# Optimization experiments

Hardware: AMD Instinct MI355X
Metric: run time of the kernel (lower is better)

Reference implementation:

```python
import jax, jax.numpy as jnp
import numpy as np

NUM_PATCHES_SIDE = 32
LOCAL_RADIUS = 3.0


def _build_non_local_mask():
    # coords of each patch on the grid, matching torch.meshgrid(indexing='ij')
    h = np.arange(NUM_PATCHES_SIDE)
    hh, ww = np.meshgrid(h, h, indexing='ij')
    coors = np.stack([hh, ww], axis=0).astype(np.float32)  # (2, H, W)
    coors = coors.reshape(2, -1).T                          # (n, 2)
    dist = np.linalg.norm(coors[:, None, :] - coors[None, :, :], axis=-1)
    return jnp.asarray(dist > LOCAL_RADIUS)                 # (n, n) bool


def setup_inputs() -> dict:
    key = jax.random.key(0)
    b, n, l, d = 8, NUM_PATCHES_SIDE * NUM_PATCHES_SIDE, 6, 512
    levels = jax.random.normal(key, (b, n, l, d), dtype=jnp.float32)
    non_local_mask = _build_non_local_mask()
    return {"levels": levels, "non_local_mask": non_local_mask}


def reference(levels, non_local_mask):
    b, n, l, d = levels.shape
    # F.normalize(levels, dim=-1): x / max(||x||, eps)
    norm = jnp.linalg.norm(levels, axis=-1, keepdims=True)
    k = levels / jnp.maximum(norm, 1e-12)
    # scores per level: (b, l, n, n)
    sim = jnp.einsum('bild,bjld->blij', levels, k) * (d ** -0.5)
    max_neg = -jnp.finfo(sim.dtype).max
    sim = jnp.where(non_local_mask[None, None, :, :], max_neg, sim)
    attn = jax.nn.softmax(sim, axis=-1)
    out = jnp.einsum('blij,bjld->bild', attn, levels)
    return out
```

## Files before the change

kernel.cpp:

```cpp
#include <hip/hip_runtime.h>
#include <math.h>

#define NPS 32
#define NN  (NPS*NPS)
#define LL  6
#define DD  512
#define ROWSPB (NN*LL)
#define BIAS 576

#define INV_SQRT_D 0.044194173824159216f
#define LOG2E      1.4426950408889634f
#define KLOG       (INV_SQRT_D * LOG2E)

__device__ __forceinline__ float half_sum32(float x) {
    int t;
    t = __builtin_amdgcn_update_dpp(0, __float_as_int(x), 0xB1, 0xF, 0xF, true);
    x += __int_as_float(t);
    t = __builtin_amdgcn_update_dpp(0, __float_as_int(x), 0x4E, 0xF, 0xF, true);
    x += __int_as_float(t);
    t = __builtin_amdgcn_update_dpp(0, __float_as_int(x), 0x141, 0xF, 0xF, true);
    x += __int_as_float(t);
    t = __builtin_amdgcn_update_dpp(0, __float_as_int(x), 0x140, 0xF, 0xF, true);
    x += __int_as_float(t);
    x += __int_as_float(__builtin_amdgcn_ds_swizzle(__float_as_int(x), 0x401F));
    return x;
}

__device__ __forceinline__ float wave_sum_bcast(float x) {
    x = half_sum32(x);
    x += __shfl_xor(x, 32, 64);
    return x;
}

__global__ __launch_bounds__(256) void ca_norm2(const float* __restrict__ levels,
                                                float* __restrict__ cws,
                                                float* __restrict__ mws, int rows) {
    int tid  = threadIdx.x;
    int lane = tid & 63;
    int sl   = lane & 31;
    int grp  = lane >> 5;
    int w = ((int)blockIdx.x * 4 + (tid >> 6)) * 2 + grp;
    if (w >= rows) return;
    const float4* x4 = (const float4*)(levels + (unsigned)(w * DD));
    float4 a0 = x4[sl], a1 = x4[sl+32], a2 = x4[sl+64], a3 = x4[sl+96];
    float s2 = a0.x*a0.x + a0.y*a0.y + a0.z*a0.z + a0.w*a0.w
             + a1.x*a1.x + a1.y*a1.y + a1.z*a1.z + a1.w*a1.w
             + a2.x*a2.x + a2.y*a2.y + a2.z*a2.z + a2.w*a2.w
             + a3.x*a3.x + a3.y*a3.y + a3.z*a3.z + a3.w*a3.w;
    s2 = half_sum32(s2);
    if (sl == 0) {
        float r = __frsqrt_rn(s2);
        cws[w] = KLOG * r;
        mws[w] = KLOG * s2 * r;
    }
}

__global__ __launch_bounds__(256) void ca_fused3(const float* __restrict__ levels,
                                                 const float* __restrict__ cws,
                                                 const float* __restrict__ mws,
                                                 float* __restrict__ out, int rows) {
    constexpr int dhA[14] = {-3,-2,-2,-1,-1,-1, 0, 0, 0, 1, 1, 2, 2, 2};
    constexpr int dwA[14] = { 0,-1, 1,-2, 0, 2,-2, 1, 3,-1, 1,-2, 0, 2};
    constexpr int dhB[14] = {-2,-2,-2,-1,-1, 0, 0, 0, 1, 1, 1, 2, 2, 3};
    constexpr int dwB[14] = {-2, 0, 2,-1, 1,-3,-1, 2,-2, 0, 2,-1, 1, 0};

    unsigned bk    = blockIdx.x;
    unsigned chunk = gridDim.x >> 3;
    unsigned vb    = (bk & 7) * chunk + (bk >> 3);

    int tid  = threadIdx.x;
    int lane = tid & 63;
    int sl   = lane & 31;
    bool hi  = lane >= 32;

    int b  = (int)(vb / 1536u);
    int r1 = (int)(vb - (unsigned)b * 1536u);
    int pg = r1 / 6;
    int l  = r1 - pg * 6;
    int p  = __builtin_amdgcn_readfirstlane(pg * 4 + (tid >> 6));
    int w  = __builtin_amdgcn_readfirstlane(b * ROWSPB + p * LL + l);
    if (w >= rows) return;
    int ph = p >> 5;
    int pw = p & 31;

    const float4* xi4 = (const float4*)(levels + (size_t)w * DD);
    float4 a0 = xi4[sl], a1 = xi4[sl+32], a2 = xi4[sl+64], a3 = xi4[sl+96];

    float m2 = mws[w];

    float  lsum = 0.0f;
    float4 c0 = make_float4(0.f,0.f,0.f,0.f);
    float4 c1 = make_float4(0.f,0.f,0.f,0.f);
    float4 c2 = make_float4(0.f,0.f,0.f,0.f);
    float4 c3 = make_float4(0.f,0.f,0.f,0.f);

    const char* lvb   = (const char*)levels + ((long long)w - BIAS) * (DD * 4);
    const char* cwb   = (const char*)cws    + ((long long)w - BIAS) * 4;

    #pragma unroll
    for (int t = 0; t < 14; ++t) {
        int hA = ph + dhA[t], wA = pw + dwA[t];
        int hB = ph + dhB[t], wB = pw + dwB[t];
        bool vA = ((unsigned)hA < NPS) && ((unsigned)wA < NPS);
        bool vB = ((unsigned)hB < NPS) && ((unsigned)wB < NPS);
        if (vA | vB) {
            int roffA = vA ? (dhA[t] * NPS + dwA[t]) * LL : 0;
            int roffB = vB ? (dhB[t] * NPS + dwB[t]) * LL : 0;
            int offA  = (roffA + BIAS) * (DD * 4);
            int offB  = (roffB + BIAS) * (DD * 4);
            int off   = hi ? offB : offA;
            const float4* bp = (const float4*)(lvb + off);
            float4 b0 = bp[sl], b1 = bp[sl+32], b2 = bp[sl+64], b3 = bp[sl+96];
            float cj = *(const float*)(cwb + (off >> 9));

            float d;
            d = a0.x * b0.x;
            d = fmaf(a0.y, b0.y, d); d = fmaf(a0.z, b0.z, d); d = fmaf(a0.w, b0.w, d);
            d = fmaf(a1.x, b1.x, d); d = fmaf(a1.y, b1.y, d); d = fmaf(a1.z, b1.z, d);
            d = fmaf(a1.w, b1.w, d);
            d = fmaf(a2.x, b2.x, d); d = fmaf(a2.y, b2.y, d); d = fmaf(a2.z, b2.z, d);
            d = fmaf(a2.w, b2.w, d);
            d = fmaf(a3.x, b3.x, d); d = fmaf(a3.y, b3.y, d); d = fmaf(a3.z, b3.z, d);
            d = fmaf(a3.w, b3.w, d);
            d = half_sum32(d);

            float pr = __builtin_amdgcn_exp2f(fmaf(d, cj, -m2));
            bool myv = hi ? vB : vA;
            pr = myv ? pr : 0.0f;
            lsum += pr;
            c0.x = fmaf(pr, b0.x, c0.x); c0.y = fmaf(pr, b0.y, c0.y);
            c0.z = fmaf(pr, b0.z, c0.z); c0.w = fmaf(pr, b0.w, c0.w);
            c1.x = fmaf(pr, b1.x, c1.x); c1.y = fmaf(pr, b1.y, c1.y);
            c1.z = fmaf(pr, b1.z, c1.z); c1.w = fmaf(pr, b1.w, c1.w);
            c2.x = fmaf(pr, b2.x, c2.x); c2.y = fmaf(pr, b2.y, c2.y);
            c2.z = fmaf(pr, b2.z, c2.z); c2.w = fmaf(pr, b2.w, c2.w);
            c3.x = fmaf(pr, b3.x, c3.x); c3.y = fmaf(pr, b3.y, c3.y);
            c3.z = fmaf(pr, b3.z, c3.z); c3.w = fmaf(pr, b3.w, c3.w);
        }
    }

    lsum += __shfl_xor(lsum, 32, 64);
    c0.x += __shfl_xor(c0.x, 32, 64); c0.y += __shfl_xor(c0.y, 32, 64);
    c0.z += __shfl_xor(c0.z, 32, 64); c0.w += __shfl_xor(c0.w, 32, 64);
    c1.x += __shfl_xor(c1.x, 32, 64); c1.y += __shfl_xor(c1.y, 32, 64);
    c1.z += __shfl_xor(c1.z, 32, 64); c1.w += __shfl_xor(c1.w, 32, 64);
    c2.x += __shfl_xor(c2.x, 32, 64); c2.y += __shfl_xor(c2.y, 32, 64);
    c2.z += __shfl_xor(c2.z, 32, 64); c2.w += __shfl_xor(c2.w, 32, 64);
    c3.x += __shfl_xor(c3.x, 32, 64); c3.y += __shfl_xor(c3.y, 32, 64);
    c3.z += __shfl_xor(c3.z, 32, 64); c3.w += __shfl_xor(c3.w, 32, 64);

    lsum += 1.0f;
    c0.x += a0.x; c0.y += a0.y; c0.z += a0.z; c0.w += a0.w;
    c1.x += a1.x; c1.y += a1.y; c1.z += a1.z; c1.w += a1.w;
    c2.x += a2.x; c2.y += a2.y; c2.z += a2.z; c2.w += a2.w;
    c3.x += a3.x; c3.y += a3.y; c3.z += a3.z; c3.w += a3.w;

    if (!hi) {
        float inv = 1.0f / lsum;
        float4* o4 = (float4*)(out + (size_t)w * DD);
        o4[sl]    = make_float4(c0.x*inv, c0.y*inv, c0.z*inv, c0.w*inv);
        o4[sl+32] = make_float4(c1.x*inv, c1.y*inv, c1.z*inv, c1.w*inv);
        o4[sl+64] = make_float4(c2.x*inv, c2.y*inv, c2.z*inv, c2.w*inv);
        o4[sl+96] = make_float4(c3.x*inv, c3.y*inv, c3.z*inv, c3.w*inv);
    }
}

__global__ __launch_bounds__(256) void ca_fallback(const float* __restrict__ levels,
                                                   float* __restrict__ out, int rows) {
    constexpr int dh[28] = {-3,-2,-2,-2,-2,-2,-1,-1,-1,-1,-1, 0, 0, 0, 0, 0, 0,
                             1, 1, 1, 1, 1, 2, 2, 2, 2, 2, 3};
    constexpr int dw[28] = { 0,-2,-1, 0, 1, 2,-2,-1, 0, 1, 2,-3,-2,-1, 1, 2, 3,
                            -2,-1, 0, 1, 2,-2,-1, 0, 1, 2, 0};
    unsigned bk    = blockIdx.x;
    unsigned chunk = gridDim.x >> 3;
    unsigned vb    = (bk & 7) * chunk + (bk >> 3);
    int w = __builtin_amdgcn_readfirstlane((int)(vb * 4 + (threadIdx.x >> 6)));
    if (w >= rows) return;
    int lane = threadIdx.x & 63;
    int i  = (w / LL) % NN;
    int ph = i >> 5, pw = i & 31;
    const float4* xi4 = (const float4*)(levels + (size_t)w * DD);
    float4 a0 = xi4[lane], a1 = xi4[lane + 64];
    float s2i = a0.x*a0.x + a0.y*a0.y + a0.z*a0.z + a0.w*a0.w
              + a1.x*a1.x + a1.y*a1.y + a1.z*a1.z + a1.w*a1.w;
    s2i = wave_sum_bcast(s2i);
    float m2 = __fsqrt_rn(s2i) * KLOG;
    float lsum = 1.0f;
    float acc0=a0.x, acc1=a0.y, acc2=a0.z, acc3=a0.w;
    float acc4=a1.x, acc5=a1.y, acc6=a1.z, acc7=a1.w;
    #pragma unroll
    for (int t = 0; t < 28; ++t) {
        int hh = ph + dh[t], ww = pw + dw[t];
        if ((unsigned)hh < (unsigned)NPS && (unsigned)ww < (unsigned)NPS) {
            int jrow = w + (dh[t] * NPS + dw[t]) * LL;
            const float4* xj4 = (const float4*)(levels + (size_t)jrow * DD);
            float4 b0 = xj4[lane], b1 = xj4[lane + 64];
            float d = a0.x * b0.x;
            d = fmaf(a0.y, b0.y, d); d = fmaf(a0.z, b0.z, d); d = fmaf(a0.w, b0.w, d);
            d = fmaf(a1.x, b1.x, d); d = fmaf(a1.y, b1.y, d); d = fmaf(a1.z, b1.z, d);
            d = fmaf(a1.w, b1.w, d);
            d = wave_sum_bcast(d);
            float q2 = b0.x*b0.x + b0.y*b0.y + b0.z*b0.z + b0.w*b0.w
                     + b1.x*b1.x + b1.y*b1.y + b1.z*b1.z + b1.w*b1.w;
            q2 = wave_sum_bcast(q2);
            float cj = KLOG * __frsqrt_rn(q2);
            float p = __builtin_amdgcn_exp2f(fmaf(d, cj, -m2));
            lsum += p;
            acc0 = fmaf(p, b0.x, acc0); acc1 = fmaf(p, b0.y, acc1);
            acc2 = fmaf(p, b0.z, acc2); acc3 = fmaf(p, b0.w, acc3);
            acc4 = fmaf(p, b1.x, acc4); acc5 = fmaf(p, b1.y, acc5);
            acc6 = fmaf(p, b1.z, acc6); acc7 = fmaf(p, b1.w, acc7);
        }
    }
    float inv = 1.0f / lsum;
    float4* o4 = (float4*)(out + (size_t)w * DD);
    o4[lane]      = make_float4(acc0*inv, acc1*inv, acc2*inv, acc3*inv);
    o4[lane + 64] = make_float4(acc4*inv, acc5*inv, acc6*inv, acc7*inv);
}

extern "C" void kernel_launch(void* const* d_in, const int* in_sizes, int n_in,
                              void* d_out, int out_size, void* d_ws, size_t ws_size,
                              hipStream_t stream) {
    const float* levels = (const float*)d_in[0];
    float* out = (float*)d_out;

    int rows = in_sizes[0] / DD;

    if (d_ws && ws_size >= (size_t)rows * 2 * sizeof(float)) {
        float* cws = (float*)d_ws;
        float* mws = cws + rows;
        int blocks1 = (rows + 7) / 8;
        ca_norm2<<<blocks1, 256, 0, stream>>>(levels, cws, mws, rows);
        int blocks2 = rows / 4;
        ca_fused3<<<blocks2, 256, 0, stream>>>(levels, cws, mws, out, rows);
    } else {
        int blocks = (rows + 3) / 4;
        ca_fallback<<<blocks, 256, 0, stream>>>(levels, out, rows);
    }
}
```

Measured before the change: 254.2 us.

## Process two horizontally adjacent query patches per wave to share neighbor loads

Each wave now handles two adjacent query rows (patches p0 and p0+1) instead of one. The neighbor loop iterates over the union of both patches' local windows, so each loaded neighbor vector is used for both queries when it lies in both windows. This halves the block count and is meant to cut redundant global/L2 reads of neighbor rows. In exchange it doubles the accumulator register footprint, which may lower occupancy, and it adds a rows%48 guard on the fast path.

```diff
diff --git a/kernel.cpp b/kernel.cpp
--- a/kernel.cpp
+++ b/kernel.cpp
@@ -30,6 +30,21 @@
     x = half_sum32(x);
     x += __shfl_xor(x, 32, 64);
     return x;
+}
+
+__device__ __forceinline__ float dot16(const float4& a0, const float4& a1,
+                                       const float4& a2, const float4& a3,
+                                       const float4& b0, const float4& b1,
+                                       const float4& b2, const float4& b3) {
+    float d = a0.x * b0.x;
+    d = fmaf(a0.y, b0.y, d); d = fmaf(a0.z, b0.z, d); d = fmaf(a0.w, b0.w, d);
+    d = fmaf(a1.x, b1.x, d); d = fmaf(a1.y, b1.y, d); d = fmaf(a1.z, b1.z, d);
+    d = fmaf(a1.w, b1.w, d);
+    d = fmaf(a2.x, b2.x, d); d = fmaf(a2.y, b2.y, d); d = fmaf(a2.z, b2.z, d);
+    d = fmaf(a2.w, b2.w, d);
+    d = fmaf(a3.x, b3.x, d); d = fmaf(a3.y, b3.y, d); d = fmaf(a3.z, b3.z, d);
+    d = fmaf(a3.w, b3.w, d);
+    return d;
 }
 
 __global__ __launch_bounds__(256) void ca_norm2(const float* __restrict__ levels,
@@ -43,10 +58,7 @@
     if (w >= rows) return;
     const float4* x4 = (const float4*)(levels + (unsigned)(w * DD));
     float4 a0 = x4[sl], a1 = x4[sl+32], a2 = x4[sl+64], a3 = x4[sl+96];
-    float s2 = a0.x*a0.x + a0.y*a0.y + a0.z*a0.z + a0.w*a0.w
-             + a1.x*a1.x + a1.y*a1.y + a1.z*a1.z + a1.w*a1.w
-             + a2.x*a2.x + a2.y*a2.y + a2.z*a2.z + a2.w*a2.w
-             + a3.x*a3.x + a3.y*a3.y + a3.z*a3.z + a3.w*a3.w;
+    float s2 = dot16(a0,a1,a2,a3, a0,a1,a2,a3);
     s2 = half_sum32(s2);
     if (sl == 0) {
         float r = __frsqrt_rn(s2);
@@ -55,14 +67,16 @@
     }
 }
 
-__global__ __launch_bounds__(256) void ca_fused3(const float* __restrict__ levels,
+__global__ __launch_bounds__(256) void ca_fused4(const float* __restrict__ levels,
                                                  const float* __restrict__ cws,
                                                  const float* __restrict__ mws,
                                                  float* __restrict__ out, int rows) {
-    constexpr int dhA[14] = {-3,-2,-2,-1,-1,-1, 0, 0, 0, 1, 1, 2, 2, 2};
-    constexpr int dwA[14] = { 0,-1, 1,-2, 0, 2,-2, 1, 3,-1, 1,-2, 0, 2};
-    constexpr int dhB[14] = {-2,-2,-2,-1,-1, 0, 0, 0, 1, 1, 1, 2, 2, 3};
-    constexpr int dwB[14] = {-2, 0, 2,-1, 1,-3,-1, 2,-2, 0, 2,-1, 1, 0};
+    constexpr int NIT = 18;
+    constexpr int typ [NIT] = { 2, 2, 2, 2, 2, 2, 2, 2, 2, 2,  0, 0, 0, 0,  1, 1, 1, 1};
+    constexpr int dhA_[NIT] = {-2,-2,-1,-1, 0, 0, 1, 1, 2, 2, -3,-2,-1, 0, -3,-2,-1, 0};
+    constexpr int duA_[NIT] = {-1, 0,-1, 0,-2,-1,-1, 0,-1, 0,  0,-2,-2,-3,  1, 3, 3, 0};
+    constexpr int dhB_[NIT] = {-2,-2,-1,-1, 0, 0, 1, 1, 2, 2,  0, 1, 2, 3,  0, 1, 2, 3};
+    constexpr int duB_[NIT] = { 1, 2, 1, 2, 2, 3, 1, 2, 1, 2,  1,-2,-2, 0,  4, 3, 3, 1};
 
     unsigned bk    = blockIdx.x;
     unsigned chunk = gridDim.x >> 3;
@@ -73,96 +87,116 @@
     int sl   = lane & 31;
     bool hi  = lane >= 32;
 
-    int b  = (int)(vb / 1536u);
-    int r1 = (int)(vb - (unsigned)b * 1536u);
+    int b  = (int)(vb / 768u);
+    int r1 = (int)(vb - (unsigned)b * 768u);
     int pg = r1 / 6;
     int l  = r1 - pg * 6;
-    int p  = __builtin_amdgcn_readfirstlane(pg * 4 + (tid >> 6));
-    int w  = __builtin_amdgcn_readfirstlane(b * ROWSPB + p * LL + l);
-    if (w >= rows) return;
-    int ph = p >> 5;
-    int pw = p & 31;
-
-    const float4* xi4 = (const float4*)(levels + (size_t)w * DD);
-    float4 a0 = xi4[sl], a1 = xi4[sl+32], a2 = xi4[sl+64], a3 = xi4[sl+96];
-
-    float m2 = mws[w];
-
-    float  lsum = 0.0f;
-    float4 c0 = make_float4(0.f,0.f,0.f,0.f);
-    float4 c1 = make_float4(0.f,0.f,0.f,0.f);
-    float4 c2 = make_float4(0.f,0.f,0.f,0.f);
-    float4 c3 = make_float4(0.f,0.f,0.f,0.f);
-
-    const char* lvb   = (const char*)levels + ((long long)w - BIAS) * (DD * 4);
-    const char* cwb   = (const char*)cws    + ((long long)w - BIAS) * 4;
+    int p0 = pg * 8 + ((tid >> 6) << 1);
+    int w0 = __builtin_amdgcn_readfirstlane(b * ROWSPB + p0 * LL + l);
+    if (w0 >= rows) return;
+    int ph  = p0 >> 5;
+    int pw0 = p0 & 31;
+
+    const float4* x0 = (const float4*)(levels + (size_t)w0 * DD);
+    const float4* x1 = x0 + (DD / 4) * LL;
+    float4 a00 = x0[sl], a01 = x0[sl+32], a02 = x0[sl+64], a03 = x0[sl+96];
+    float4 a10 = x1[sl], a11 = x1[sl+32], a12 = x1[sl+64], a13 = x1[sl+96];
+
+    float m20 = mws[w0];
+    float m21 = mws[w0 + LL];
+
+    float  lsum0 = 0.0f, lsum1 = 0.0f;
+    float4 c00 = make_float4(0,0,0,0), c01 = make_float4(0,0,0,0);
+    float4 c02 = make_float4(0,0,0,0), c03 = make_float4(0,0,0,0);
+    float4 c10 = make_float4(0,0,0,0), c11 = make_float4(0,0,0,0);
+    float4 c12 = make_float4(0,0,0,0), c13 = make_float4(0,0,0,0);
+
+    const char* lvb = (const char*)levels + ((long long)w0 - BIAS) * (DD * 4);
+    const char* cwb = (const char*)cws    + ((long long)w0 - BIAS) * 4;
 
     #pragma unroll
-    for (int t = 0; t < 14; ++t) {
-        int hA = ph + dhA[t], wA = pw + dwA[t];
-        int hB = ph + dhB[t], wB = pw + dwB[t];
-        bool vA = ((unsigned)hA < NPS) && ((unsigned)wA < NPS);
-        bool vB = ((unsigned)hB < NPS) && ((unsigned)wB < NPS);
-        if (vA | vB) {
-            int roffA = vA ? (dhA[t] * NPS + dwA[t]) * LL : 0;
-            int roffB = vB ? (dhB[t] * NPS + dwB[t]) * LL : 0;
-            int offA  = (roffA + BIAS) * (DD * 4);
-            int offB  = (roffB + BIAS) * (DD * 4);
-            int off   = hi ? offB : offA;
-            const float4* bp = (const float4*)(lvb + off);
-            float4 b0 = bp[sl], b1 = bp[sl+32], b2 = bp[sl+64], b3 = bp[sl+96];
-            float cj = *(const float*)(cwb + (off >> 9));
-
-            float d;
-            d = a0.x * b0.x;
-            d = fmaf(a0.y, b0.y, d); d = fmaf(a0.z, b0.z, d); d = fmaf(a0.w, b0.w, d);
-            d = fmaf(a1.x, b1.x, d); d = fmaf(a1.y, b1.y, d); d = fmaf(a1.z, b1.z, d);
-            d = fmaf(a1.w, b1.w, d);
-            d = fmaf(a2.x, b2.x, d); d = fmaf(a2.y, b2.y, d); d = fmaf(a2.z, b2.z, d);
-            d = fmaf(a2.w, b2.w, d);
-            d = fmaf(a3.x, b3.x, d); d = fmaf(a3.y, b3.y, d); d = fmaf(a3.z, b3.z, d);
-            d = fmaf(a3.w, b3.w, d);
-            d = half_sum32(d);
-
-            float pr = __builtin_amdgcn_exp2f(fmaf(d, cj, -m2));
-            bool myv = hi ? vB : vA;
-            pr = myv ? pr : 0.0f;
-            lsum += pr;
-            c0.x = fmaf(pr, b0.x, c0.x); c0.y = fmaf(pr, b0.y, c0.y);
-            c0.z = fmaf(pr, b0.z, c0.z); c0.w = fmaf(pr, b0.w, c0.w);
-            c1.x = fmaf(pr, b1.x, c1.x); c1.y = fmaf(pr, b1.y, c1.y);
-            c1.z = fmaf(pr, b1.z, c1.z); c1.w = fmaf(pr, b1.w, c1.w);
-            c2.x = fmaf(pr, b2.x, c2.x); c2.y = fmaf(pr, b2.y, c2.y);
-            c2.z = fmaf(pr, b2.z, c2.z); c2.w = fmaf(pr, b2.w, c2.w);
-            c3.x = fmaf(pr, b3.x, c3.x); c3.y = fmaf(pr, b3.y, c3.y);
-            c3.z = fmaf(pr, b3.z, c3.z); c3.w = fmaf(pr, b3.w, c3.w);
+    for (int t = 0; t < NIT; ++t) {
+        const int dA = dhA_[t], uA = duA_[t];
+        const int dB = dhB_[t], uB = duB_[t];
+        bool vA = ((unsigned)(ph + dA) < (unsigned)NPS) &&
+                  ((unsigned)(pw0 + uA) < (unsigned)NPS);
+        bool vB = ((unsigned)(ph + dB) < (unsigned)NPS) &&
+                  ((unsigned)(pw0 + uB) < (unsigned)NPS);
+        int offA = ((vA ? (dA * NPS + uA) * LL : 0) + BIAS) * (DD * 4);
+        int offB = ((vB ? (dB * NPS + uB) * LL : 0) + BIAS) * (DD * 4);
+        int off  = hi ? offB : offA;
+        const char* bp = lvb + off;
+        float4 b0 = *(const float4*)(bp + sl * 16);
+        float4 b1 = *(const float4*)(bp + sl * 16 + 512);
+        float4 b2 = *(const float4*)(bp + sl * 16 + 1024);
+        float4 b3 = *(const float4*)(bp + sl * 16 + 1536);
+        float  cj = *(const float*)(cwb + (off >> 9));
+        float  vm = (hi ? vB : vA) ? 1.0f : 0.0f;
+
+        float d0 = 0.f, d1 = 0.f;
+        if (typ[t] != 1) d0 = dot16(a00,a01,a02,a03, b0,b1,b2,b3);
+        if (typ[t] != 0) d1 = dot16(a10,a11,a12,a13, b0,b1,b2,b3);
+        if (typ[t] != 1) d0 = half_sum32(d0);
+        if (typ[t] != 0) d1 = half_sum32(d1);
+
+        if (typ[t] != 1) {
+            float pr0 = vm * __builtin_amdgcn_exp2f(fmaf(d0, cj, -m20));
+            lsum0 += pr0;
+            c00.x = fmaf(pr0, b0.x, c00.x); c00.y = fmaf(pr0, b0.y, c00.y);
+            c00.z = fmaf(pr0, b0.z, c00.z); c00.w = fmaf(pr0, b0.w, c00.w);
+            c01.x = fmaf(pr0, b1.x, c01.x); c01.y = fmaf(pr0, b1.y, c01.y);
+            c01.z = fmaf(pr0, b1.z, c01.z); c01.w = fmaf(pr0, b1.w, c01.w);
+            c02.x = fmaf(pr0, b2.x, c02.x); c02.y = fmaf(pr0, b2.y, c02.y);
+            c02.z = fmaf(pr0, b2.z, c02.z); c02.w = fmaf(pr0, b2.w, c02.w);
+            c03.x = fmaf(pr0, b3.x, c03.x); c03.y = fmaf(pr0, b3.y, c03.y);
+            c03.z = fmaf(pr0, b3.z, c03.z); c03.w = fmaf(pr0, b3.w, c03.w);
         }
-    }
-
-    lsum += __shfl_xor(lsum, 32, 64);
-    c0.x += __shfl_xor(c0.x, 32, 64); c0.y += __shfl_xor(c0.y, 32, 64);
-    c0.z += __shfl_xor(c0.z, 32, 64); c0.w += __shfl_xor(c0.w, 32, 64);
-    c1.x += __shfl_xor(c1.x, 32, 64); c1.y += __shfl_xor(c1.y, 32, 64);
-    c1.z += __shfl_xor(c1.z, 32, 64); c1.w += __shfl_xor(c1.w, 32, 64);
-    c2.x += __shfl_xor(c2.x, 32, 64); c2.y += __shfl_xor(c2.y, 32, 64);
-    c2.z += __shfl_xor(c2.z, 32, 64); c2.w += __shfl_xor(c2.w, 32, 64);
-    c3.x += __shfl_xor(c3.x, 32, 64); c3.y += __shfl_xor(c3.y, 32, 64);
-    c3.z += __shfl_xor(c3.z, 32, 64); c3.w += __shfl_xor(c3.w, 32, 64);
-
-    lsum += 1.0f;
-    c0.x += a0.x; c0.y += a0.y; c0.z += a0.z; c0.w += a0.w;
-    c1.x += a1.x; c1.y += a1.y; c1.z += a1.z; c1.w += a1.w;
-    c2.x += a2.x; c2.y += a2.y; c2.z += a2.z; c2.w += a2.w;
-    c3.x += a3.x; c3.y += a3.y; c3.z += a3.z; c3.w += a3.w;
-
-    if (!hi) {
-        float inv = 1.0f / lsum;
-        float4* o4 = (float4*)(out + (size_t)w * DD);
-        o4[sl]    = make_float4(c0.x*inv, c0.y*inv, c0.z*inv, c0.w*inv);
-        o4[sl+32] = make_float4(c1.x*inv, c1.y*inv, c1.z*inv, c1.w*inv);
-        o4[sl+64] = make_float4(c2.x*inv, c2.y*inv, c2.z*inv, c2.w*inv);
-        o4[sl+96] = make_float4(c3.x*inv, c3.y*inv, c3.z*inv, c3.w*inv);
-    }
+        if (typ[t] != 0) {
+            float pr1 = vm * __builtin_amdgcn_exp2f(fmaf(d1, cj, -m21));
+            lsum1 += pr1;
+            c10.x = fmaf(pr1, b0.x, c10.x); c10.y = fmaf(pr1, b0.y, c10.y);
+            c10.z = fmaf(pr1, b0.z, c10.z); c10.w = fmaf(pr1, b0.w, c10.w);
+            c11.x = fmaf(pr1, b1.x, c11.x); c11.y = fmaf(pr1, b1.y, c11.y);
+            c11.z = fmaf(pr1, b1.z, c11.z); c11.w = fmaf(pr1, b1.w, c11.w);
+            c12.x = fmaf(pr1, b2.x, c12.x); c12.y = fmaf(pr1, b2.y, c12.y);
+            c12.z = fmaf(pr1, b2.z, c12.z); c12.w = fmaf(pr1, b2.w, c12.w);
+            c13.x = fmaf(pr1, b3.x, c13.x); c13.y = fmaf(pr1, b3.y, c13.y);
+            c13.z = fmaf(pr1, b3.z, c13.z); c13.w = fmaf(pr1, b3.w, c13.w);
+        }
+    }
+
+    #define CMB(v) v += __shfl_xor(v, 32, 64)
+    CMB(lsum0); CMB(lsum1);
+    CMB(c00.x); CMB(c00.y); CMB(c00.z); CMB(c00.w);
+    CMB(c01.x); CMB(c01.y); CMB(c01.z); CMB(c01.w);
+    CMB(c02.x); CMB(c02.y); CMB(c02.z); CMB(c02.w);
+    CMB(c03.x); CMB(c03.y); CMB(c03.z); CMB(c03.w);
+    CMB(c10.x); CMB(c10.y); CMB(c10.z); CMB(c10.w);
+    CMB(c11.x); CMB(c11.y); CMB(c11.z); CMB(c11.w);
+    CMB(c12.x); CMB(c12.y); CMB(c12.z); CMB(c12.w);
+    CMB(c13.x); CMB(c13.y); CMB(c13.z); CMB(c13.w);
+    #undef CMB
+
+    lsum0 += 1.0f; lsum1 += 1.0f;
+    c00.x += a00.x; c00.y += a00.y; c00.z += a00.z; c00.w += a00.w;
+    c01.x += a01.x; c01.y += a01.y; c01.z += a01.z; c01.w += a01.w;
+    c02.x += a02.x; c02.y += a02.y; c02.z += a02.z; c02.w += a02.w;
+    c03.x += a03.x; c03.y += a03.y; c03.z += a03.z; c03.w += a03.w;
+    c10.x += a10.x; c10.y += a10.y; c10.z += a10.z; c10.w += a10.w;
+    c11.x += a11.x; c11.y += a11.y; c11.z += a11.z; c11.w += a11.w;
+    c12.x += a12.x; c12.y += a12.y; c12.z += a12.z; c12.w += a12.w;
+    c13.x += a13.x; c13.y += a13.y; c13.z += a13.z; c13.w += a13.w;
+
+    float  inv = 1.0f / (hi ? lsum1 : lsum0);
+    float4 s0 = hi ? c10 : c00;
+    float4 s1 = hi ? c11 : c01;
+    float4 s2 = hi ? c12 : c02;
+    float4 s3 = hi ? c13 : c03;
+    float4* o4 = (float4*)(out + (size_t)(hi ? w0 + LL : w0) * DD);
+    o4[sl]    = make_float4(s0.x*inv, s0.y*inv, s0.z*inv, s0.w*inv);
+    o4[sl+32] = make_float4(s1.x*inv, s1.y*inv, s1.z*inv, s1.w*inv);
+    o4[sl+64] = make_float4(s2.x*inv, s2.y*inv, s2.z*inv, s2.w*inv);
+    o4[sl+96] = make_float4(s3.x*inv, s3.y*inv, s3.z*inv, s3.w*inv);
 }
 
 __global__ __launch_bounds__(256) void ca_fallback(const float* __restrict__ levels,
@@ -226,13 +260,13 @@
 
     int rows = in_sizes[0] / DD;
 
-    if (d_ws && ws_size >= (size_t)rows * 2 * sizeof(float)) {
+    if (d_ws && ws_size >= (size_t)rows * 2 * sizeof(float) && (rows % 48) == 0) {
         float* cws = (float*)d_ws;
         float* mws = cws + rows;
         int blocks1 = (rows + 7) / 8;
         ca_norm2<<<blocks1, 256, 0, stream>>>(levels, cws, mws, rows);
-        int blocks2 = rows / 4;
-        ca_fused3<<<blocks2, 256, 0, stream>>>(levels, cws, mws, out, rows);
+        int blocks2 = rows / 8;
+        ca_fused4<<<blocks2, 256, 0, stream>>>(levels, cws, mws, out, rows);
     } else {
         int blocks = (rows + 3) / 4;
         ca_fallback<<<blocks, 256, 0, stream>>>(levels, out, rows);
```

After: 235.1 us. 1.08x faster.
